# Optimization experiments

Measured on AMD Instinct MI355X. Metric: run time of the kernel, lower is better.

## Reference

```python
import jax, jax.numpy as jnp
import numpy as np

D_MODEL = 1024
HEADS = 16
D_K = D_MODEL // HEADS
B, S = 2, 2048
NEG = -1000000000.0

def setup_inputs() -> dict:
    key = jax.random.key(0)
    ks = jax.random.split(key, 11)
    sc = 1.0 / np.sqrt(D_MODEL)
    inp = {
        'q': jax.random.normal(ks[0], (B, S, D_MODEL), jnp.float32),
        'k': jax.random.normal(ks[1], (B, S, D_MODEL), jnp.float32),
        'v': jax.random.normal(ks[2], (B, S, D_MODEL), jnp.float32),
        'mask': jnp.tril(jnp.ones((S, S), jnp.int32))[None, None],  # causal [1,1,S,S]
        'wq_w': jax.random.normal(ks[3], (D_MODEL, D_MODEL), jnp.float32) * sc,
        'wq_b': jax.random.normal(ks[4], (D_MODEL,), jnp.float32) * 0.02,
        'wk_w': jax.random.normal(ks[5], (D_MODEL, D_MODEL), jnp.float32) * sc,
        'wk_b': jax.random.normal(ks[6], (D_MODEL,), jnp.float32) * 0.02,
        'wv_w': jax.random.normal(ks[7], (D_MODEL, D_MODEL), jnp.float32) * sc,
        'wv_b': jax.random.normal(ks[8], (D_MODEL,), jnp.float32) * 0.02,
        'wo_w': jax.random.normal(ks[9], (D_MODEL, D_MODEL), jnp.float32) * sc,
        'wo_b': jax.random.normal(ks[10], (D_MODEL,), jnp.float32) * 0.02,
    }
    return inp

def reference(q, k, v, mask, wq_w, wq_b, wk_w, wk_b, wv_w, wv_b, wo_w, wo_b):
    b, s, _ = q.shape
    # projections (torch Linear: x @ W^T + b)
    Q = (q @ wq_w.T + wq_b).reshape(b, s, HEADS, D_K).transpose(0, 2, 1, 3)  # [B,H,S,Dk]
    K = (k @ wk_w.T + wk_b).reshape(b, s, HEADS, D_K).transpose(0, 2, 1, 3)
    V = (v @ wv_w.T + wv_b).reshape(b, s, HEADS, D_K).transpose(0, 2, 1, 3)
    scores = jnp.einsum('bhqd,bhkd->bhqk', Q, K) / jnp.sqrt(jnp.float32(D_K))
    scores = jnp.where(mask == 0, NEG, scores)
    p = jax.nn.softmax(scores, axis=-1)  # dropout=0.0 -> identity
    x = jnp.einsum('bhqk,bhkd->bhqd', p, V)
    x = x.transpose(0, 2, 1, 3).reshape(b, s, D_MODEL)
    return x @ wo_w.T + wo_b
```

## Files before the change

kernel.cpp:

```cpp
#include <hip/hip_runtime.h>

typedef unsigned short u16;
typedef __attribute__((ext_vector_type(8))) short bf16x8;
typedef __attribute__((ext_vector_type(4))) float f32x4;

#define SEQ 2048
#define DMODEL 1024

__device__ __forceinline__ u16 f2bf(float f) {
    union { float f; unsigned u; } x; x.f = f;
    unsigned r = x.u + 0x7fffu + ((x.u >> 16) & 1u);
    return (u16)(r >> 16);
}

__device__ __forceinline__ float bf2f(u16 v) {
    union { unsigned u; float f; } x; x.u = ((unsigned)v) << 16;
    return x.f;
}

__device__ __forceinline__ float fast_exp2(float x) {
    float y;
    asm("v_exp_f32 %0, %1" : "=v"(y) : "v"(x));
    return y;
}

__device__ __forceinline__ unsigned cvt_pk_bf16(float lo, float hi) {
    unsigned d;
    asm("v_cvt_pk_bf16_f32 %0, %1, %2" : "=v"(d) : "v"(lo), "v"(hi));
    return d;
}

__device__ __forceinline__ f32x4 mfma16(bf16x8 a, bf16x8 b, f32x4 c) {
    return __builtin_amdgcn_mfma_f32_16x16x32_bf16(a, b, c, 0, 0, 0);
}

__device__ __forceinline__ void gld16(const u16* g, u16* l) {
    __builtin_amdgcn_global_load_lds(
        (__attribute__((address_space(1))) const void*)g,
        (__attribute__((address_space(3))) void*)l, 16, 0, 0);
}

struct CvtArgs {
    const float* src[7];
    u16* dst[7];
    int n4[7];
};

__global__ __launch_bounds__(256) void cvt_kernel(CvtArgs a) {
    const int id = blockIdx.y;
    const int i = blockIdx.x * 256 + threadIdx.x;
    if (i >= a.n4[id]) return;
    float4 f = ((const float4*)a.src[id])[i];
    ushort4 u;
    u.x = f2bf(f.x); u.y = f2bf(f.y); u.z = f2bf(f.z); u.w = f2bf(f.w);
    ((ushort4*)a.dst[id])[i] = u;
}

__global__ __launch_bounds__(256, 4) void gemm_qkv(
    const u16* __restrict__ Xq, const u16* __restrict__ Xk, const u16* __restrict__ Xv,
    const u16* __restrict__ Wq, const u16* __restrict__ Wk, const u16* __restrict__ Wv,
    const float* __restrict__ bq, const float* __restrict__ bk, const float* __restrict__ bv,
    u16* __restrict__ Qb, u16* __restrict__ Kb, u16* __restrict__ Vb)
{
    __shared__ u16 Abuf[2][128 * 32];
    __shared__ u16 Bbuf[2][128 * 32];

    const int bid = blockIdx.x;
    const int gm = (bid & 7) * 96 + (bid >> 3);
    const int z = gm >> 8;
    const int rem = gm & 255;
    const int bm = (rem >> 3) * 128;
    const int bn = (rem & 7) * 128;

    const u16* X = (z == 0) ? Xq : (z == 1) ? Xk : Xv;
    const u16* W = (z == 0) ? Wq : (z == 1) ? Wk : Wv;
    const float* bias = (z == 0) ? bq : (z == 1) ? bk : bv;

    const int tid = threadIdx.x;
    const int lane = tid & 63, w = tid >> 6;
    const int wm = (w >> 1) * 64, wn = (w & 1) * 64;
    const int r = lane & 15, qd = lane >> 4;

    const int srow = lane >> 2;
    const int scol = (lane & 3) * 8;
    const u16* Xs = X + (size_t)(bm + w * 32 + srow) * 1024 + scol;
    const u16* Ws = W + (size_t)(bn + w * 32 + srow) * 1024 + scol;

    f32x4 acc[4][4];
    #pragma unroll
    for (int i = 0; i < 4; ++i)
        #pragma unroll
        for (int j = 0; j < 4; ++j)
            acc[i][j] = (f32x4){0.f, 0.f, 0.f, 0.f};

    auto stage = [&](int t) {
        const int d = t & 1;
        #pragma unroll
        for (int q = 0; q < 2; ++q) {
            gld16(Xs + (size_t)q * 16384 + t * 32, &Abuf[d][w * 1024 + q * 512]);
            gld16(Ws + (size_t)q * 16384 + t * 32, &Bbuf[d][w * 1024 + q * 512]);
        }
    };

    stage(0);
    stage(1);
    asm volatile("s_waitcnt vmcnt(4)" ::: "memory");
    __builtin_amdgcn_sched_barrier(0);
    __builtin_amdgcn_s_barrier();

    for (int t = 0; t < 32; ++t) {
        const u16* Ab = Abuf[t & 1];
        const u16* Bb = Bbuf[t & 1];
        bf16x8 aF[4], bF[4];
        #pragma unroll
        for (int i = 0; i < 4; ++i)
            aF[i] = *(const bf16x8*)(Ab + (wm + i * 16 + r) * 32 + qd * 8);
        #pragma unroll
        for (int j = 0; j < 4; ++j)
            bF[j] = *(const bf16x8*)(Bb + (wn + j * 16 + r) * 32 + qd * 8);
        __builtin_amdgcn_s_setprio(1);
        #pragma unroll
        for (int i = 0; i < 4; ++i)
            #pragma unroll
            for (int j = 0; j < 4; ++j)
                acc[i][j] = mfma16(aF[i], bF[j], acc[i][j]);
        __builtin_amdgcn_s_setprio(0);
        if (t == 31) break;
        asm volatile("s_waitcnt lgkmcnt(0)" ::: "memory");
        __builtin_amdgcn_sched_barrier(0);
        __builtin_amdgcn_s_barrier();
        if (t < 30) {
            stage(t + 2);
            asm volatile("s_waitcnt vmcnt(4)" ::: "memory");
        } else {
            asm volatile("s_waitcnt vmcnt(0)" ::: "memory");
        }
        __builtin_amdgcn_sched_barrier(0);
        __builtin_amdgcn_s_barrier();
        __builtin_amdgcn_sched_barrier(0);
    }

    const float scale = (z == 0) ? 0.18033688011112042f : 1.0f;
    #pragma unroll
    for (int j = 0; j < 4; ++j) {
        const int n = bn + wn + j * 16 + r;
        const float bvl = bias[n];
        const int h = n >> 6, d = n & 63;
        #pragma unroll
        for (int i = 0; i < 4; ++i) {
            const int m0 = bm + wm + i * 16 + qd * 4;
            const int b_ = m0 >> 11, s0 = m0 & 2047;
            if (z == 0) {
                #pragma unroll
                for (int reg = 0; reg < 4; ++reg)
                    Qb[(size_t)(m0 + reg) * 1024 + n] = f2bf((acc[i][j][reg] + bvl) * scale);
            } else if (z == 1) {
                #pragma unroll
                for (int reg = 0; reg < 4; ++reg)
                    Kb[((size_t)(b_ * 16 + h) * SEQ + s0 + reg) * 64 + d] =
                        f2bf(acc[i][j][reg] + bvl);
            } else {
                ushort4 u;
                u.x = f2bf(acc[i][j][0] + bvl);
                u.y = f2bf(acc[i][j][1] + bvl);
                u.z = f2bf(acc[i][j][2] + bvl);
                u.w = f2bf(acc[i][j][3] + bvl);
                *(ushort4*)(Vb + ((size_t)(b_ * 16 + h) * 64 + d) * SEQ + s0) = u;
            }
        }
    }
}

__global__ __launch_bounds__(128, 4) void attn_kernel(
    const u16* __restrict__ Qb, const u16* __restrict__ Kb,
    const u16* __restrict__ Vb, u16* __restrict__ Op, float* __restrict__ Lp)
{
    __shared__ u16 Kst[2][2048];
    __shared__ u16 Vst[2][2048];
    __shared__ u16 Pst[2][16 * 40];

    const int bid = blockIdx.x;
    const int xcd = bid & 7;
    const int i2 = bid >> 3;
    const int bh = xcd + 8 * (i2 & 3);
    const int rest = i2 >> 2;
    const int gidx = rest / 3;
    const int third = rest - gidx * 3;
    const int g = 31 - gidx;
    const int b_ = bh >> 4, h = bh & 15;

    const int n = 2 * g + 2;
    const int j0 = (n * third) / 3;
    const int j1 = (n * (third + 1)) / 3;

    const int tid = threadIdx.x;
    const int lane = tid & 63, w = tid >> 6;
    const int r = lane & 15, qd = lane >> 4;

    const u16* Kh = Kb + (size_t)bh * SEQ * 64;
    const u16* Vh = Vb + (size_t)bh * 64 * SEQ;
    u16* Pw = Pst[w];

    bf16x8 aQ[2][2];
    #pragma unroll
    for (int i = 0; i < 2; ++i) {
        const size_t qoff =
            (size_t)(b_ * SEQ + g * 64 + w * 32 + i * 16 + r) * DMODEL + h * 64;
        aQ[i][0] = *(const bf16x8*)(Qb + qoff + qd * 8);
        aQ[i][1] = *(const bf16x8*)(Qb + qoff + 32 + qd * 8);
    }

    bf16x8 ones;
    #pragma unroll
    for (int e = 0; e < 8; ++e) ones[e] = (short)0x3F80;

    f32x4 o[2][4];
    f32x4 l[2];
    #pragma unroll
    for (int i = 0; i < 2; ++i) {
        l[i] = (f32x4){0.f, 0.f, 0.f, 0.f};
        #pragma unroll
        for (int db = 0; db < 4; ++db) o[i][db] = (f32x4){0.f, 0.f, 0.f, 0.f};
    }

    auto stage = [&](int j, int buf) {
        if (w == 0) {
            const u16* Kt = Kh + (size_t)j * 32 * 64;
            #pragma unroll
            for (int s = 0; s < 4; ++s)
                gld16(Kt + ((s >> 1) * 16 + r) * 64 + (s & 1) * 32 + qd * 8,
                      &Kst[buf][s * 512]);
        } else {
            const u16* Vt = Vh + j * 32;
            #pragma unroll
            for (int s = 0; s < 4; ++s)
                gld16(Vt + (size_t)(s * 16 + r) * SEQ + qd * 8,
                      &Vst[buf][s * 512]);
        }
    };

    if (j0 < j1) {
        stage(j0, j0 & 1);
        if (j0 + 1 < j1) stage(j0 + 1, (j0 + 1) & 1);
    }

    const f32x4 shift = (f32x4){-23.083120654223414f, -23.083120654223414f,
                                -23.083120654223414f, -23.083120654223414f};

    for (int j = j0; j < j1; ++j) {
        const int cur = j & 1;
        if (j + 1 < j1) {
            asm volatile("s_waitcnt vmcnt(4)" ::: "memory");
        } else {
            asm volatile("s_waitcnt vmcnt(0)" ::: "memory");
        }
        __builtin_amdgcn_sched_barrier(0);
        __builtin_amdgcn_s_barrier();

        bf16x8 kf[2][2], vf[4];
        #pragma unroll
        for (int nb = 0; nb < 2; ++nb) {
            kf[nb][0] = *(const bf16x8*)(&Kst[cur][(nb * 2 + 0) * 512 + lane * 8]);
            kf[nb][1] = *(const bf16x8*)(&Kst[cur][(nb * 2 + 1) * 512 + lane * 8]);
        }
        #pragma unroll
        for (int db = 0; db < 4; ++db)
            vf[db] = *(const bf16x8*)(&Vst[cur][db * 512 + lane * 8]);

        #pragma unroll
        for (int i = 0; i < 2; ++i) {
            f32x4 sc[2];
            #pragma unroll
            for (int nb = 0; nb < 2; ++nb) {
                f32x4 s = shift;
                s = mfma16(kf[nb][0], aQ[i][0], s);
                s = mfma16(kf[nb][1], aQ[i][1], s);
                sc[nb] = s;
            }

            if (j >= 2 * g) {
                const int lim = g * 64 + w * 32 + i * 16 + r - j * 32;
                #pragma unroll
                for (int nb = 0; nb < 2; ++nb)
                    #pragma unroll
                    for (int reg = 0; reg < 4; ++reg)
                        if (nb * 16 + qd * 4 + reg > lim) sc[nb][reg] = -1e30f;
            }

            #pragma unroll
            for (int nb = 0; nb < 2; ++nb)
                #pragma unroll
                for (int reg = 0; reg < 4; ++reg)
                    sc[nb][reg] = fast_exp2(sc[nb][reg]);

            #pragma unroll
            for (int nb = 0; nb < 2; ++nb) {
                uint2 pk2;
                pk2.x = cvt_pk_bf16(sc[nb][0], sc[nb][1]);
                pk2.y = cvt_pk_bf16(sc[nb][2], sc[nb][3]);
                *(uint2*)(Pw + r * 40 + nb * 16 + qd * 4) = pk2;
            }

            const bf16x8 aP = *(const bf16x8*)(Pw + r * 40 + qd * 8);

            l[i] = mfma16(aP, ones, l[i]);
            #pragma unroll
            for (int db = 0; db < 4; ++db)
                o[i][db] = mfma16(aP, vf[db], o[i][db]);
        }

        if (j + 1 == j1) break;
        asm volatile("s_waitcnt lgkmcnt(0)" ::: "memory");
        __builtin_amdgcn_sched_barrier(0);
        __builtin_amdgcn_s_barrier();
        if (j + 2 < j1) stage(j + 2, cur);
        __builtin_amdgcn_sched_barrier(0);
    }

    u16* Oh = Op + ((size_t)(third * 1024 + bh * 32 + g) * 4096);
    float* Lh = Lp + (size_t)(third * 1024 + bh * 32 + g) * 64;
    #pragma unroll
    for (int i = 0; i < 2; ++i) {
        #pragma unroll
        for (int db = 0; db < 4; ++db)
            #pragma unroll
            for (int reg = 0; reg < 4; ++reg)
                Oh[(w * 32 + i * 16 + qd * 4 + reg) * 64 + db * 16 + r] =
                    f2bf(o[i][db][reg]);
        if (r == 0) {
            #pragma unroll
            for (int reg = 0; reg < 4; ++reg)
                Lh[w * 32 + i * 16 + qd * 4 + reg] = l[i][reg];
        }
    }
}

__global__ __launch_bounds__(256) void attn_norm(
    const u16* __restrict__ Op, const float* __restrict__ Lp,
    u16* __restrict__ AO)
{
    const int idx = blockIdx.x * 256 + threadIdx.x;
    const int col8 = idx & 127;
    const int row = idx >> 7;
    const int h = col8 >> 3;
    const int b_ = row >> 11, s = row & 2047;
    const int g = s >> 6, r64 = s & 63;
    const int bh = b_ * 16 + h;

    const size_t pa = ((size_t)(bh * 32 + g) * 4096) + r64 * 64 + (col8 & 7) * 8;
    const size_t pb = pa + (size_t)1024 * 4096;
    const size_t pc = pb + (size_t)1024 * 4096;
    const float la = Lp[(bh * 32 + g) * 64 + r64];
    const float lb = Lp[(1024 + bh * 32 + g) * 64 + r64];
    const float lc = Lp[(2048 + bh * 32 + g) * 64 + r64];
    const float inv = 1.0f / (la + lb + lc);

    const bf16x8 a = *(const bf16x8*)(Op + pa);
    const bf16x8 b = *(const bf16x8*)(Op + pb);
    const bf16x8 c = *(const bf16x8*)(Op + pc);
    bf16x8 o;
    #pragma unroll
    for (int e = 0; e < 8; ++e)
        o[e] = (short)f2bf((bf2f((u16)a[e]) + bf2f((u16)b[e]) + bf2f((u16)c[e])) * inv);
    *(bf16x8*)(AO + (size_t)row * 1024 + col8 * 8) = o;
}

__global__ __launch_bounds__(256, 4) void gemm_out(
    const u16* __restrict__ AO, const u16* __restrict__ W,
    const float* __restrict__ bias, float* __restrict__ out)
{
    __shared__ u16 Abuf[2][64 * 32];
    __shared__ u16 Bbuf[2][128 * 32];

    const int bid = blockIdx.x;
    const int gm = (bid & 7) * 64 + (bid >> 3);
    const int bm = (gm >> 3) * 64;
    const int bn = (gm & 7) * 128;

    const int tid = threadIdx.x;
    const int lane = tid & 63, w = tid >> 6;
    const int wm = (w >> 1) * 32, wn = (w & 1) * 64;
    const int r = lane & 15, qd = lane >> 4;

    const int srow = lane >> 2;
    const int scol = (lane & 3) * 8;
    const u16* Xs = AO + (size_t)(bm + w * 16 + srow) * 1024 + scol;
    const u16* Ws = W + (size_t)(bn + w * 32 + srow) * 1024 + scol;

    f32x4 acc[2][4];
    #pragma unroll
    for (int i = 0; i < 2; ++i)
        #pragma unroll
        for (int j = 0; j < 4; ++j)
            acc[i][j] = (f32x4){0.f, 0.f, 0.f, 0.f};

    auto stage = [&](int t) {
        const int d = t & 1;
        gld16(Xs + t * 32, &Abuf[d][w * 512]);
        #pragma unroll
        for (int q = 0; q < 2; ++q)
            gld16(Ws + (size_t)q * 16384 + t * 32, &Bbuf[d][w * 1024 + q * 512]);
    };

    stage(0);
    stage(1);
    asm volatile("s_waitcnt vmcnt(3)" ::: "memory");
    __builtin_amdgcn_sched_barrier(0);
    __builtin_amdgcn_s_barrier();

    for (int t = 0; t < 32; ++t) {
        const u16* Ab = Abuf[t & 1];
        const u16* Bb = Bbuf[t & 1];
        bf16x8 aF[2], bF[4];
        #pragma unroll
        for (int i = 0; i < 2; ++i)
            aF[i] = *(const bf16x8*)(Ab + (wm + i * 16 + r) * 32 + qd * 8);
        #pragma unroll
        for (int j = 0; j < 4; ++j)
            bF[j] = *(const bf16x8*)(Bb + (wn + j * 16 + r) * 32 + qd * 8);
        __builtin_amdgcn_s_setprio(1);
        #pragma unroll
        for (int i = 0; i < 2; ++i)
            #pragma unroll
            for (int j = 0; j < 4; ++j)
                acc[i][j] = mfma16(aF[i], bF[j], acc[i][j]);
        __builtin_amdgcn_s_setprio(0);
        if (t == 31) break;
        asm volatile("s_waitcnt lgkmcnt(0)" ::: "memory");
        __builtin_amdgcn_sched_barrier(0);
        __builtin_amdgcn_s_barrier();
        if (t < 30) {
            stage(t + 2);
            asm volatile("s_waitcnt vmcnt(3)" ::: "memory");
        } else {
            asm volatile("s_waitcnt vmcnt(0)" ::: "memory");
        }
        __builtin_amdgcn_sched_barrier(0);
        __builtin_amdgcn_s_barrier();
        __builtin_amdgcn_sched_barrier(0);
    }

    #pragma unroll
    for (int j = 0; j < 4; ++j) {
        const int n = bn + wn + j * 16 + r;
        const float bvl = bias[n];
        #pragma unroll
        for (int i = 0; i < 2; ++i) {
            const int m0 = bm + wm + i * 16 + qd * 4;
            #pragma unroll
            for (int reg = 0; reg < 4; ++reg)
                out[(size_t)(m0 + reg) * 1024 + n] = acc[i][j][reg] + bvl;
        }
    }
}

extern "C" void kernel_launch(void* const* d_in, const int* in_sizes, int n_in,
                              void* d_out, int out_size, void* d_ws, size_t ws_size,
                              hipStream_t stream) {
    const float* q  = (const float*)d_in[0];
    const float* k  = (const float*)d_in[1];
    const float* v  = (const float*)d_in[2];
    const float* wq = (const float*)d_in[4];
    const float* bq = (const float*)d_in[5];
    const float* wk = (const float*)d_in[6];
    const float* bk = (const float*)d_in[7];
    const float* wv = (const float*)d_in[8];
    const float* bv = (const float*)d_in[9];
    const float* wo = (const float*)d_in[10];
    const float* bo = (const float*)d_in[11];
    float* out = (float*)d_out;

    u16* ws = (u16*)d_ws;
    u16* Xq = ws;
    u16* Xk = Xq + (size_t)4194304;
    u16* Xv = Xk + (size_t)4194304;
    u16* Wq = Xv + (size_t)4194304;
    u16* Wk = Wq + (size_t)1048576;
    u16* Wv = Wk + (size_t)1048576;
    u16* Wo = Wv + (size_t)1048576;
    u16* Qb = Wo + (size_t)1048576;
    u16* Kb = Qb + (size_t)4194304;
    u16* Vb = Kb + (size_t)4194304;
    u16* AO = Vb + (size_t)4194304;

    u16* Op = ws;
    float* Lp = (float*)(ws + (size_t)12582912);

    CvtArgs ca;
    ca.src[0] = q;  ca.dst[0] = Xq; ca.n4[0] = 1048576;
    ca.src[1] = k;  ca.dst[1] = Xk; ca.n4[1] = 1048576;
    ca.src[2] = v;  ca.dst[2] = Xv; ca.n4[2] = 1048576;
    ca.src[3] = wq; ca.dst[3] = Wq; ca.n4[3] = 262144;
    ca.src[4] = wk; ca.dst[4] = Wk; ca.n4[4] = 262144;
    ca.src[5] = wv; ca.dst[5] = Wv; ca.n4[5] = 262144;
    ca.src[6] = wo; ca.dst[6] = Wo; ca.n4[6] = 262144;

    cvt_kernel<<<dim3(4096, 7), 256, 0, stream>>>(ca);
    gemm_qkv<<<dim3(768), 256, 0, stream>>>(Xq, Xk, Xv, Wq, Wk, Wv,
                                            bq, bk, bv, Qb, Kb, Vb);
    attn_kernel<<<dim3(3072), 128, 0, stream>>>(Qb, Kb, Vb, Op, Lp);
    attn_norm<<<dim3(2048), 256, 0, stream>>>(Op, Lp, AO);
    gemm_out<<<dim3(512), 256, 0, stream>>>(AO, Wo, bo, out);
}
```

Before: 233.3 us.

## Fuse split-KV attention combine into output projection GEMM A-tile load

```diff
diff --git a/kernel.cpp b/kernel.cpp
--- a/kernel.cpp
+++ b/kernel.cpp
@@ -335,42 +335,13 @@
     }
 }
 
-__global__ __launch_bounds__(256) void attn_norm(
+__global__ __launch_bounds__(256, 4) void gemm_out(
     const u16* __restrict__ Op, const float* __restrict__ Lp,
-    u16* __restrict__ AO)
-{
-    const int idx = blockIdx.x * 256 + threadIdx.x;
-    const int col8 = idx & 127;
-    const int row = idx >> 7;
-    const int h = col8 >> 3;
-    const int b_ = row >> 11, s = row & 2047;
-    const int g = s >> 6, r64 = s & 63;
-    const int bh = b_ * 16 + h;
-
-    const size_t pa = ((size_t)(bh * 32 + g) * 4096) + r64 * 64 + (col8 & 7) * 8;
-    const size_t pb = pa + (size_t)1024 * 4096;
-    const size_t pc = pb + (size_t)1024 * 4096;
-    const float la = Lp[(bh * 32 + g) * 64 + r64];
-    const float lb = Lp[(1024 + bh * 32 + g) * 64 + r64];
-    const float lc = Lp[(2048 + bh * 32 + g) * 64 + r64];
-    const float inv = 1.0f / (la + lb + lc);
-
-    const bf16x8 a = *(const bf16x8*)(Op + pa);
-    const bf16x8 b = *(const bf16x8*)(Op + pb);
-    const bf16x8 c = *(const bf16x8*)(Op + pc);
-    bf16x8 o;
-    #pragma unroll
-    for (int e = 0; e < 8; ++e)
-        o[e] = (short)f2bf((bf2f((u16)a[e]) + bf2f((u16)b[e]) + bf2f((u16)c[e])) * inv);
-    *(bf16x8*)(AO + (size_t)row * 1024 + col8 * 8) = o;
-}
-
-__global__ __launch_bounds__(256, 4) void gemm_out(
-    const u16* __restrict__ AO, const u16* __restrict__ W,
+    const u16* __restrict__ W,
     const float* __restrict__ bias, float* __restrict__ out)
 {
-    __shared__ u16 Abuf[2][64 * 32];
-    __shared__ u16 Bbuf[2][128 * 32];
+    __shared__ u16 As[64 * 32];
+    __shared__ u16 Bs[128 * 32];
 
     const int bid = blockIdx.x;
     const int gm = (bid & 7) * 64 + (bid >> 3);
@@ -384,7 +355,12 @@
 
     const int srow = lane >> 2;
     const int scol = (lane & 3) * 8;
-    const u16* Xs = AO + (size_t)(bm + w * 16 + srow) * 1024 + scol;
+
+    const int row = bm + w * 16 + srow;
+    const int b_ = row >> 11, s = row & 2047;
+    const int g = s >> 6, r64 = s & 63;
+    u16* Ad = As + (w * 16 + srow) * 32 + scol;
+
     const u16* Ws = W + (size_t)(bn + w * 32 + srow) * 1024 + scol;
 
     f32x4 acc[2][4];
@@ -394,30 +370,41 @@
         for (int j = 0; j < 4; ++j)
             acc[i][j] = (f32x4){0.f, 0.f, 0.f, 0.f};
 
-    auto stage = [&](int t) {
-        const int d = t & 1;
-        gld16(Xs + t * 32, &Abuf[d][w * 512]);
+    for (int t = 0; t < 32; ++t) {
+        __syncthreads();
+
+        {
+            const int colglob = t * 32 + scol;
+            const int h = colglob >> 6, d = colglob & 63;
+            const int bh = b_ * 16 + h;
+            const size_t base = ((size_t)(bh * 32 + g)) * 4096 + r64 * 64 + d;
+            const int lidx = (bh * 32 + g) * 64 + r64;
+
+            const bf16x8 a = *(const bf16x8*)(Op + base);
+            const bf16x8 b = *(const bf16x8*)(Op + base + (size_t)4194304);
+            const bf16x8 c = *(const bf16x8*)(Op + base + (size_t)8388608);
+            const float inv = 1.0f / (Lp[lidx] + Lp[65536 + lidx] +
+                                      Lp[131072 + lidx]);
+            bf16x8 o8;
+            #pragma unroll
+            for (int e = 0; e < 8; ++e)
+                o8[e] = (short)f2bf((bf2f((u16)a[e]) + bf2f((u16)b[e]) +
+                                     bf2f((u16)c[e])) * inv);
+            *(bf16x8*)Ad = o8;
+        }
         #pragma unroll
         for (int q = 0; q < 2; ++q)
-            gld16(Ws + (size_t)q * 16384 + t * 32, &Bbuf[d][w * 1024 + q * 512]);
-    };
-
-    stage(0);
-    stage(1);
-    asm volatile("s_waitcnt vmcnt(3)" ::: "memory");
-    __builtin_amdgcn_sched_barrier(0);
-    __builtin_amdgcn_s_barrier();
-
-    for (int t = 0; t < 32; ++t) {
-        const u16* Ab = Abuf[t & 1];
-        const u16* Bb = Bbuf[t & 1];
+            gld16(Ws + (size_t)q * 16384 + t * 32, Bs + w * 1024 + q * 512);
+
+        __syncthreads();
+
         bf16x8 aF[2], bF[4];
         #pragma unroll
         for (int i = 0; i < 2; ++i)
-            aF[i] = *(const bf16x8*)(Ab + (wm + i * 16 + r) * 32 + qd * 8);
+            aF[i] = *(const bf16x8*)(As + (wm + i * 16 + r) * 32 + qd * 8);
         #pragma unroll
         for (int j = 0; j < 4; ++j)
-            bF[j] = *(const bf16x8*)(Bb + (wn + j * 16 + r) * 32 + qd * 8);
+            bF[j] = *(const bf16x8*)(Bs + (wn + j * 16 + r) * 32 + qd * 8);
         __builtin_amdgcn_s_setprio(1);
         #pragma unroll
         for (int i = 0; i < 2; ++i)
@@ -425,19 +412,6 @@
             for (int j = 0; j < 4; ++j)
                 acc[i][j] = mfma16(aF[i], bF[j], acc[i][j]);
         __builtin_amdgcn_s_setprio(0);
-        if (t == 31) break;
-        asm volatile("s_waitcnt lgkmcnt(0)" ::: "memory");
-        __builtin_amdgcn_sched_barrier(0);
-        __builtin_amdgcn_s_barrier();
-        if (t < 30) {
-            stage(t + 2);
-            asm volatile("s_waitcnt vmcnt(3)" ::: "memory");
-        } else {
-            asm volatile("s_waitcnt vmcnt(0)" ::: "memory");
-        }
-        __builtin_amdgcn_sched_barrier(0);
-        __builtin_amdgcn_s_barrier();
-        __builtin_amdgcn_sched_barrier(0);
     }
 
     #pragma unroll
@@ -481,7 +455,6 @@
     u16* Qb = Wo + (size_t)1048576;
     u16* Kb = Qb + (size_t)4194304;
     u16* Vb = Kb + (size_t)4194304;
-    u16* AO = Vb + (size_t)4194304;
 
     u16* Op = ws;
     float* Lp = (float*)(ws + (size_t)12582912);
@@ -499,6 +472,5 @@
     gemm_qkv<<<dim3(768), 256, 0, stream>>>(Xq, Xk, Xv, Wq, Wk, Wv,
                                             bq, bk, bv, Qb, Kb, Vb);
     attn_kernel<<<dim3(3072), 128, 0, stream>>>(Qb, Kb, Vb, Op, Lp);
-    attn_norm<<<dim3(2048), 256, 0, stream>>>(Op, Lp, AO);
-    gemm_out<<<dim3(512), 256, 0, stream>>>(AO, Wo, bo, out);
-}
+    gemm_out<<<dim3(512), 256, 0, stream>>>(Op, Lp, Wo, bo, out);
+}
```

New measurement: 238.6 us. 2.3% more time.
